# Kernel optimization log

Hardware: AMD Instinct MI355X
Metric: run time of the kernel (lower is better)

The kernel has to match this reference:

```python
import jax, jax.numpy as jnp
import numpy as np

C = 512        # concept_num
D = 256        # input_dim / embedding_dim
H = 512        # msg_hidden_dim
M = 256        # msg_output_dim
OH = 512       # hidden_dim
T = 2          # edge_type_num
E = C * (C - 1)  # fully-connected graph without self-loops = 261632


def _glorot(key, shape, fan_in):
    return jax.random.normal(key, shape, jnp.float32) / np.sqrt(fan_in).astype(np.float32)


def setup_inputs() -> dict:
    key = jax.random.key(0)
    ks = jax.random.split(key, 12)
    inputs = jax.random.normal(ks[0], (C, D), jnp.float32)
    rel_type = jax.random.uniform(ks[1], (E, T), jnp.float32)
    send_idx = jax.random.randint(ks[2], (E,), 0, C, jnp.int32)
    rec_idx = jax.random.randint(ks[3], (E,), 0, C, jnp.int32)
    # per-edge-type message MLP params, stacked over type dim
    W1 = _glorot(ks[4], (T, 2 * D, H), 2 * D)
    b1 = jnp.zeros((T, H), jnp.float32)
    W2 = _glorot(ks[5], (T, H, M), H)
    b2 = jnp.zeros((T, M), jnp.float32)
    # output MLP params
    Wo1 = _glorot(ks[6], (M, OH), M)
    bo1 = jnp.zeros((OH,), jnp.float32)
    Wo2 = _glorot(ks[7], (OH, OH), OH)
    bo2 = jnp.zeros((OH,), jnp.float32)
    Wo3 = _glorot(ks[8], (OH, D), OH)
    bo3 = jnp.zeros((D,), jnp.float32)
    return {"inputs": inputs, "rel_type": rel_type, "W1": W1, "b1": b1,
            "W2": W2, "b2": b2, "Wo1": Wo1, "bo1": bo1, "Wo2": Wo2,
            "bo2": bo2, "Wo3": Wo3, "bo3": bo3,
            "send_idx": send_idx, "rec_idx": rec_idx}


def reference(inputs, rel_type, W1, b1, W2, b2, Wo1, bo1, Wo2, bo2, Wo3, bo3,
              send_idx, rec_idx):
    # node2edge: one-hot sparse matmul == index gather
    senders = jnp.take(inputs, send_idx, axis=0)      # [E, D]
    receivers = jnp.take(inputs, rec_idx, axis=0)     # [E, D]
    pre_msg = jnp.concatenate([senders, receivers], axis=-1)  # [E, 2D]
    # per-edge-type MLPs, weighted-summed by rel_type (dropout=0 / eval mode)
    all_msgs = jnp.zeros((pre_msg.shape[0], M), jnp.float32)
    for i in range(T):
        msg = jax.nn.relu(pre_msg @ W1[i] + b1[i])    # [E, H]
        msg = jax.nn.relu(msg @ W2[i] + b2[i])        # [E, M]
        all_msgs = all_msgs + msg * rel_type[:, i:i + 1]
    # edge2node: transposed one-hot sparse matmul == scatter-add over receivers
    agg_msgs = jax.ops.segment_sum(all_msgs, rec_idx, num_segments=inputs.shape[0])  # [C, M]
    pred = jax.nn.relu(agg_msgs @ Wo1 + bo1)
    pred = jax.nn.relu(pred @ Wo2 + bo2)
    return pred @ Wo3 + bo3                           # [C, D]
```

## Files before the change

kernel.cpp:

```cpp
#include <hip/hip_runtime.h>

#define C_N   512
#define E_N   261632

typedef _Float16 f16;
typedef _Float16 f16x8_t __attribute__((ext_vector_type(8)));
typedef float    f32x16_t __attribute__((ext_vector_type(16)));

__global__ __launch_bounds__(256) void k_prep(
    const float* __restrict__ W1, const float* __restrict__ W2,
    const int* __restrict__ rec,
    const float* __restrict__ Wo1, const float* __restrict__ Wo2, const float* __restrict__ Wo3,
    f16* __restrict__ W1p, f16* __restrict__ W2p,
    f16* __restrict__ Wo1p, f16* __restrict__ Wo2p, f16* __restrict__ Wo3p,
    int* __restrict__ hist_part)
{
  int bid = blockIdx.x;
  if (bid < 256) {
    int gid  = bid * 256 + threadIdx.x;
    int lane = gid & 63;
    int nt   = (gid >> 6) & 15;
    int kc   = (gid >> 10) & 15;
    int mi   = gid >> 14;
    int t    = mi >> 1, half = mi & 1;
    const float* src = W1 + (size_t)t * 512 * 512 + (size_t)half * 256 * 512;
    int n  = nt * 32 + (lane & 31);
    int k0 = kc * 16 + (lane >> 5) * 8;
    f16x8_t v;
    #pragma unroll
    for (int j = 0; j < 8; j++) v[j] = (f16)src[(size_t)(k0 + j) * 512 + n];
    *(f16x8_t*)(W1p + (size_t)gid * 8) = v;
  } else if (bid < 384) {
    int gid  = (bid - 256) * 256 + threadIdx.x;
    int lane = gid & 63;
    int ct   = (gid >> 6) & 7;
    int kc   = (gid >> 9) & 31;
    int t    = gid >> 14;
    int n    = ct * 32 + (lane & 31);
    int k0   = kc * 16 + (lane >> 5) * 8;
    const float* src = W2 + (size_t)t * 512 * 256;
    f16x8_t v;
    #pragma unroll
    for (int j = 0; j < 8; j++) v[j] = (f16)src[(size_t)(k0 + j) * 256 + n];
    *(f16x8_t*)(W2p + (size_t)gid * 8) = v;
  } else if (bid < 448) {
    int hb = bid - 384;
    __shared__ int lh[512];
    for (int i = threadIdx.x; i < 512; i += 256) lh[i] = 0;
    __syncthreads();
    int e0 = hb * (E_N / 64);
    for (int i = threadIdx.x; i < E_N / 64; i += 256)
      atomicAdd(&lh[rec[e0 + i]], 1);
    __syncthreads();
    for (int i = threadIdx.x; i < 512; i += 256)
      hist_part[hb * 512 + i] = lh[i];
  } else if (bid < 512) {
    int gid  = (bid - 448) * 256 + threadIdx.x;
    int lane = gid & 63;
    int ct   = (gid >> 6) & 15;
    int kc   = gid >> 10;
    int n    = ct * 32 + (lane & 31);
    int k0   = kc * 16 + (lane >> 5) * 8;
    f16x8_t v;
    #pragma unroll
    for (int j = 0; j < 8; j++) v[j] = (f16)Wo1[(size_t)(k0 + j) * 512 + n];
    *(f16x8_t*)(Wo1p + (size_t)gid * 8) = v;
  } else if (bid < 640) {
    int gid  = (bid - 512) * 256 + threadIdx.x;
    int lane = gid & 63;
    int ct   = (gid >> 6) & 15;
    int kc   = gid >> 10;
    int n    = ct * 32 + (lane & 31);
    int k0   = kc * 16 + (lane >> 5) * 8;
    f16x8_t v;
    #pragma unroll
    for (int j = 0; j < 8; j++) v[j] = (f16)Wo2[(size_t)(k0 + j) * 512 + n];
    *(f16x8_t*)(Wo2p + (size_t)gid * 8) = v;
  } else {
    int gid  = (bid - 640) * 256 + threadIdx.x;
    int lane = gid & 63;
    int ct   = (gid >> 6) & 7;
    int kc   = gid >> 9;
    int n    = ct * 32 + (lane & 31);
    int k0   = kc * 16 + (lane >> 5) * 8;
    f16x8_t v;
    #pragma unroll
    for (int j = 0; j < 8; j++) v[j] = (f16)Wo3[(size_t)(k0 + j) * 256 + n];
    *(f16x8_t*)(Wo3p + (size_t)gid * 8) = v;
  }
}

__global__ __launch_bounds__(256) void k_sarb(const float* __restrict__ inputs,
    const f16* __restrict__ W1p, const float* __restrict__ b1,
    f16* __restrict__ SA, f16* __restrict__ RB)
{
  int tid = threadIdx.x, lane = tid & 63, w = tid >> 6;
  int hlf = lane >> 5, l31 = lane & 31;
  int br = blockIdx.x, bc = blockIdx.y, mi = blockIdx.z;
  int t = mi >> 1, half = mi & 1;
  const f16* Bmat = W1p + (size_t)mi * (256 * 512);
  f32x16_t acc[2][2];
  #pragma unroll
  for (int rt = 0; rt < 2; rt++)
    #pragma unroll
    for (int ctl = 0; ctl < 2; ctl++)
      #pragma unroll
      for (int r = 0; r < 16; r++) acc[rt][ctl][r] = 0.f;
  for (int kc = 0; kc < 16; kc++) {
    f16x8_t af[2];
    #pragma unroll
    for (int rt = 0; rt < 2; rt++) {
      const float4* p = (const float4*)&inputs[(size_t)(br * 64 + rt * 32 + l31) * 256 + kc * 16 + hlf * 8];
      float4 u0 = p[0], u1 = p[1];
      af[rt] = (f16x8_t){(f16)u0.x, (f16)u0.y, (f16)u0.z, (f16)u0.w,
                         (f16)u1.x, (f16)u1.y, (f16)u1.z, (f16)u1.w};
    }
    #pragma unroll
    for (int ctl = 0; ctl < 2; ctl++) {
      f16x8_t bfr = *(const f16x8_t*)&Bmat[((size_t)(kc * 16 + bc * 8 + 2 * w + ctl) * 64 + lane) * 8];
      #pragma unroll
      for (int rt = 0; rt < 2; rt++)
        acc[rt][ctl] = __builtin_amdgcn_mfma_f32_32x32x16_f16(af[rt], bfr, acc[rt][ctl], 0, 0, 0);
    }
  }
  f16* dst = (half == 0) ? SA : RB;
  #pragma unroll
  for (int ctl = 0; ctl < 2; ctl++) {
    int col = bc * 256 + (2 * w + ctl) * 32 + l31;
    float bias = (half == 1) ? b1[t * 512 + col] : 0.f;
    #pragma unroll
    for (int rt = 0; rt < 2; rt++)
      #pragma unroll
      for (int r = 0; r < 16; r++) {
        int row = br * 64 + rt * 32 + (r & 3) + 8 * (r >> 2) + 4 * hlf;
        dst[((size_t)(t * 512 + row)) * 512 + col] = (f16)(acc[rt][ctl][r] + bias);
      }
  }
}

__global__ void k_scan(const int* __restrict__ hist_part, int* __restrict__ seg,
                       int* __restrict__ base)
{
  __shared__ int s[512];
  int tid = threadIdx.x;
  int tot = 0;
  #pragma unroll 8
  for (int b = 0; b < 64; b++) tot += hist_part[b * 512 + tid];
  s[tid] = tot;
  __syncthreads();
  for (int off = 1; off < 512; off <<= 1) {
    int v = (tid >= off) ? s[tid - off] : 0;
    __syncthreads();
    s[tid] += v;
    __syncthreads();
  }
  int excl = s[tid] - tot;
  seg[tid] = excl;
  if (tid == 0) seg[512] = E_N;
  int run = excl;
  for (int b = 0; b < 64; b++) {
    base[b * 512 + tid] = run;
    run += hist_part[b * 512 + tid];
  }
}

__global__ __launch_bounds__(1024) void k_scatter3(const int* __restrict__ rec,
    const int* __restrict__ send, const float* __restrict__ rel,
    const int* __restrict__ base, int* __restrict__ ssend, float2* __restrict__ srel)
{
  __shared__ int lh[512];
  __shared__ int lb[512];
  int b = blockIdx.x;
  int e0 = b * (E_N / 64);
  for (int i = threadIdx.x; i < 512; i += 1024) { lh[i] = 0; lb[i] = base[b * 512 + i]; }
  __syncthreads();
  for (int i = threadIdx.x; i < E_N / 64; i += 1024) {
    int e = e0 + i;
    int r = rec[e];
    int p = lb[r] + atomicAdd(&lh[r], 1);
    ssend[p] = send[e];
    srel[p]  = make_float2(rel[2 * (size_t)e], rel[2 * (size_t)e + 1]);
  }
}

#define H1S2 264

__global__ __launch_bounds__(512, 4) void k_edges(
    const f16* __restrict__ SA, const f16* __restrict__ RB,
    const f16* __restrict__ W2p, const float* __restrict__ b2,
    const int* __restrict__ ssend, const float2* __restrict__ srel,
    const int* __restrict__ seg, float* __restrict__ agg)
{
  __shared__ f16   h1[128 * H1S2];
  __shared__ f16   rbs[2][512];
  __shared__ float b2s[2][256];
  __shared__ float aggL[256];
  __shared__ float relv2[2][128][2];
  __shared__ int   sends2[2][128];

  int c    = blockIdx.x;
  int tid  = threadIdx.x;
  int lane = tid & 63;
  int w    = tid >> 6;
  int hlf  = lane >> 5;
  int l31  = lane & 31;
  int q5   = tid & 31;
  int rb0  = tid >> 5;

  if (tid < 128) {
    int t = tid >> 6, qq = tid & 63;
    *(f16x8_t*)&rbs[t][qq * 8] = *(const f16x8_t*)&RB[((size_t)(t * 512 + c)) * 512 + qq * 8];
  }
  if (tid < 256) aggL[tid] = 0.0f;
  { int t = (tid >> 8) & 1, col = tid & 255; b2s[t][col] = b2[t * 256 + col]; }

  int s0 = seg[c], s1 = seg[c + 1];
  int nt = (s1 - s0 + 127) >> 7;

  if (nt > 0 && tid < 128) {
    int pos = s0 + tid;
    if (pos < s1) {
      sends2[0][tid] = ssend[pos];
      float2 rr = srel[pos];
      relv2[0][tid][0] = rr.x;
      relv2[0][tid][1] = rr.y;
    } else {
      sends2[0][tid] = 0; relv2[0][tid][0] = 0.f; relv2[0][tid][1] = 0.f;
    }
  }
  __syncthreads();

  f16x8_t g[8];
  const f16x8_t* SAc = (const f16x8_t*)SA;
  const f16x8_t* Bp  = (const f16x8_t*)W2p;
  f32x16_t acc[4];

  if (nt > 0) {
    #pragma unroll
    for (int j = 0; j < 8; j++)
      g[j] = SAc[(size_t)sends2[0][rb0 + 16 * j] * 64 + q5];
  }

  for (int ph = 0; ph < 4 * nt; ph++) {
    int ti  = ph >> 2;
    int t   = (ph >> 1) & 1;
    int kh  = ph & 1;
    int cb  = ti & 1;
    int nb  = cb ^ 1;
    bool more = (ti + 1 < nt);

    {
      f16x8_t rbq = *(const f16x8_t*)&rbs[t][(kh * 32 + q5) * 8];
      #pragma unroll
      for (int j = 0; j < 8; j++) {
        int row = rb0 + 16 * j;
        f16x8_t hv;
        #pragma unroll
        for (int e = 0; e < 8; e++) {
          f16 v = (f16)(g[j][e] + rbq[e]);
          hv[e] = (v > (f16)0.0f) ? v : (f16)0.0f;
        }
        *(f16x8_t*)&h1[row * H1S2 + q5 * 8] = hv;
      }
    }
    __syncthreads();

    if (t == 0 && kh == 0 && more && tid < 128) {
      int pos = s0 + (ti + 1) * 128 + tid;
      if (pos < s1) {
        sends2[nb][tid] = ssend[pos];
        float2 rr = srel[pos];
        relv2[nb][tid][0] = rr.x;
        relv2[nb][tid][1] = rr.y;
      } else {
        sends2[nb][tid] = 0; relv2[nb][tid][0] = 0.f; relv2[nb][tid][1] = 0.f;
      }
    }

    if (kh == 0) {
      #pragma unroll
      for (int rt = 0; rt < 4; rt++)
        #pragma unroll
        for (int r = 0; r < 16; r++) acc[rt][r] = 0.f;
    }

    f16x8_t bb[2];
    bb[0] = Bp[(size_t)(((t * 32 + kh * 16 + 0) * 8 + w) * 64 + lane)];
    bb[1] = Bp[(size_t)(((t * 32 + kh * 16 + 1) * 8 + w) * 64 + lane)];

    if (kh == 0) {
      #pragma unroll
      for (int j = 0; j < 8; j++)
        g[j] = SAc[(size_t)(t * 512 + sends2[cb][rb0 + 16 * j]) * 64 + 32 + q5];
    } else if (t == 0) {
      #pragma unroll
      for (int j = 0; j < 8; j++)
        g[j] = SAc[(size_t)(512 + sends2[cb][rb0 + 16 * j]) * 64 + q5];
    } else if (more) {
      #pragma unroll
      for (int j = 0; j < 8; j++)
        g[j] = SAc[(size_t)sends2[nb][rb0 + 16 * j] * 64 + q5];
    }

    for (int kc = 0; kc < 16; kc++) {
      int pb = kc & 1;
      #pragma unroll
      for (int rt = 0; rt < 4; rt++) {
        f16x8_t af = *(const f16x8_t*)&h1[(rt * 32 + l31) * H1S2 + kc * 16 + hlf * 8];
        acc[rt] = __builtin_amdgcn_mfma_f32_32x32x16_f16(af, bb[pb], acc[rt], 0, 0, 0);
      }
      if (kc + 2 < 16)
        bb[pb] = Bp[(size_t)(((t * 32 + kh * 16 + kc + 2) * 8 + w) * 64 + lane)];
    }

    if (kh == 1) {
      int col = w * 32 + l31;
      float b2c = b2s[t][col];
      float csum = 0.0f;
      #pragma unroll
      for (int rt = 0; rt < 4; rt++)
        #pragma unroll
        for (int r = 0; r < 16; r++) {
          int row = rt * 32 + (r & 3) + 8 * (r >> 2) + 4 * hlf;
          float v = fmaxf(acc[rt][r] + b2c, 0.0f);
          csum += v * relv2[cb][row][t];
        }
      csum += __shfl_xor(csum, 32, 64);
      if (hlf == 0) aggL[col] += csum;
    }
    __syncthreads();
  }

  if (tid < 256) agg[(size_t)c * 256 + tid] = aggL[tid];
}

__global__ __launch_bounds__(256) void k_omlp1(const float* __restrict__ agg,
    const f16* __restrict__ Wo1p, const float* __restrict__ bo1, f16* __restrict__ h1o)
{
  int tid = threadIdx.x, lane = tid & 63, w = tid >> 6;
  int hlf = lane >> 5, l31 = lane & 31;
  int br = blockIdx.x, bc = blockIdx.y;
  f32x16_t acc[2][2];
  #pragma unroll
  for (int rt = 0; rt < 2; rt++)
    #pragma unroll
    for (int ctl = 0; ctl < 2; ctl++)
      #pragma unroll
      for (int r = 0; r < 16; r++) acc[rt][ctl][r] = 0.f;
  for (int kc = 0; kc < 16; kc++) {
    f16x8_t af[2];
    #pragma unroll
    for (int rt = 0; rt < 2; rt++) {
      const float4* p = (const float4*)&agg[(size_t)(br * 64 + rt * 32 + l31) * 256 + kc * 16 + hlf * 8];
      float4 u0 = p[0], u1 = p[1];
      af[rt] = (f16x8_t){(f16)u0.x, (f16)u0.y, (f16)u0.z, (f16)u0.w,
                         (f16)u1.x, (f16)u1.y, (f16)u1.z, (f16)u1.w};
    }
    #pragma unroll
    for (int ctl = 0; ctl < 2; ctl++) {
      f16x8_t bfr = *(const f16x8_t*)&Wo1p[((size_t)(kc * 16 + bc * 8 + 2 * w + ctl) * 64 + lane) * 8];
      #pragma unroll
      for (int rt = 0; rt < 2; rt++)
        acc[rt][ctl] = __builtin_amdgcn_mfma_f32_32x32x16_f16(af[rt], bfr, acc[rt][ctl], 0, 0, 0);
    }
  }
  #pragma unroll
  for (int ctl = 0; ctl < 2; ctl++) {
    int col = bc * 256 + (2 * w + ctl) * 32 + l31;
    float bias = bo1[col];
    #pragma unroll
    for (int rt = 0; rt < 2; rt++)
      #pragma unroll
      for (int r = 0; r < 16; r++) {
        int row = br * 64 + rt * 32 + (r & 3) + 8 * (r >> 2) + 4 * hlf;
        h1o[(size_t)row * 512 + col] = (f16)fmaxf(acc[rt][ctl][r] + bias, 0.f);
      }
  }
}

__global__ __launch_bounds__(256) void k_omlp2(const f16* __restrict__ h1o,
    const f16* __restrict__ Wo2p, const float* __restrict__ bo2, f16* __restrict__ h2o)
{
  int tid = threadIdx.x, lane = tid & 63, w = tid >> 6;
  int hlf = lane >> 5, l31 = lane & 31;
  int br = blockIdx.x, bc = blockIdx.y;
  f32x16_t acc[2][2];
  #pragma unroll
  for (int rt = 0; rt < 2; rt++)
    #pragma unroll
    for (int ctl = 0; ctl < 2; ctl++)
      #pragma unroll
      for (int r = 0; r < 16; r++) acc[rt][ctl][r] = 0.f;
  for (int kc = 0; kc < 32; kc++) {
    f16x8_t af[2];
    #pragma unroll
    for (int rt = 0; rt < 2; rt++)
      af[rt] = *(const f16x8_t*)&h1o[(size_t)(br * 64 + rt * 32 + l31) * 512 + kc * 16 + hlf * 8];
    #pragma unroll
    for (int ctl = 0; ctl < 2; ctl++) {
      f16x8_t bfr = *(const f16x8_t*)&Wo2p[((size_t)(kc * 16 + bc * 8 + 2 * w + ctl) * 64 + lane) * 8];
      #pragma unroll
      for (int rt = 0; rt < 2; rt++)
        acc[rt][ctl] = __builtin_amdgcn_mfma_f32_32x32x16_f16(af[rt], bfr, acc[rt][ctl], 0, 0, 0);
    }
  }
  #pragma unroll
  for (int ctl = 0; ctl < 2; ctl++) {
    int col = bc * 256 + (2 * w + ctl) * 32 + l31;
    float bias = bo2[col];
    #pragma unroll
    for (int rt = 0; rt < 2; rt++)
      #pragma unroll
      for (int r = 0; r < 16; r++) {
        int row = br * 64 + rt * 32 + (r & 3) + 8 * (r >> 2) + 4 * hlf;
        h2o[(size_t)row * 512 + col] = (f16)fmaxf(acc[rt][ctl][r] + bias, 0.f);
      }
  }
}

__global__ __launch_bounds__(256) void k_omlp3(const f16* __restrict__ h2o,
    const f16* __restrict__ Wo3p, const float* __restrict__ bo3, float* __restrict__ out)
{
  int tid = threadIdx.x, lane = tid & 63, w = tid >> 6;
  int hlf = lane >> 5, l31 = lane & 31;
  int br = blockIdx.x;
  f32x16_t acc[2][2];
  #pragma unroll
  for (int rt = 0; rt < 2; rt++)
    #pragma unroll
    for (int ctl = 0; ctl < 2; ctl++)
      #pragma unroll
      for (int r = 0; r < 16; r++) acc[rt][ctl][r] = 0.f;
  for (int kc = 0; kc < 32; kc++) {
    f16x8_t af[2];
    #pragma unroll
    for (int rt = 0; rt < 2; rt++)
      af[rt] = *(const f16x8_t*)&h2o[(size_t)(br * 64 + rt * 32 + l31) * 512 + kc * 16 + hlf * 8];
    #pragma unroll
    for (int ctl = 0; ctl < 2; ctl++) {
      f16x8_t bfr = *(const f16x8_t*)&Wo3p[((size_t)(kc * 8 + 2 * w + ctl) * 64 + lane) * 8];
      #pragma unroll
      for (int rt = 0; rt < 2; rt++)
        acc[rt][ctl] = __builtin_amdgcn_mfma_f32_32x32x16_f16(af[rt], bfr, acc[rt][ctl], 0, 0, 0);
    }
  }
  #pragma unroll
  for (int ctl = 0; ctl < 2; ctl++) {
    int col = (2 * w + ctl) * 32 + l31;
    float bias = bo3[col];
    #pragma unroll
    for (int rt = 0; rt < 2; rt++)
      #pragma unroll
      for (int r = 0; r < 16; r++) {
        int row = br * 64 + rt * 32 + (r & 3) + 8 * (r >> 2) + 4 * hlf;
        out[(size_t)row * 256 + col] = acc[rt][ctl][r] + bias;
      }
  }
}

extern "C" void kernel_launch(void* const* d_in, const int* in_sizes, int n_in,
                              void* d_out, int out_size, void* d_ws, size_t ws_size,
                              hipStream_t stream)
{
  (void)in_sizes; (void)n_in; (void)out_size; (void)ws_size;
  const float* inputs = (const float*)d_in[0];
  const float* rel    = (const float*)d_in[1];
  const float* W1     = (const float*)d_in[2];
  const float* b1     = (const float*)d_in[3];
  const float* W2     = (const float*)d_in[4];
  const float* b2     = (const float*)d_in[5];
  const float* Wo1    = (const float*)d_in[6];
  const float* bo1    = (const float*)d_in[7];
  const float* Wo2    = (const float*)d_in[8];
  const float* bo2    = (const float*)d_in[9];
  const float* Wo3    = (const float*)d_in[10];
  const float* bo3    = (const float*)d_in[11];
  const int* send_idx = (const int*)d_in[12];
  const int* rec_idx  = (const int*)d_in[13];
  float* out = (float*)d_out;

  char* ws = (char*)d_ws;
  f16*    SA        = (f16*)   (ws);
  f16*    RB        = (f16*)   (ws + (1u << 20));
  f16*    W2p       = (f16*)   (ws + (2u << 20));
  float*  agg       = (float*) (ws + (2560u << 10));
  int*    hist_part = (int*)   (ws + (3u << 20));
  int*    seg       = (int*)   (ws + (3u << 20) + (128u << 10));
  int*    base      = (int*)   (ws + (3u << 20) + (132u << 10));
  int*    ssend     = (int*)   (ws + (3584u << 10));
  float2* srel      = (float2*)(ws + (4608u << 10));
  f16*    Wo1p      = (f16*)   (ws + (6656u << 10));
  f16*    Wo2p      = (f16*)   (ws + (6912u << 10));
  f16*    Wo3p      = (f16*)   (ws + (7424u << 10));
  f16*    h1o       = (f16*)   (ws + (7680u << 10));
  f16*    h2o       = (f16*)   (ws + (8192u << 10));
  f16*    W1p       = (f16*)   (ws + (8704u << 10));

  k_prep    <<<dim3(704),     dim3(256),  0, stream>>>(W1, W2, rec_idx, Wo1, Wo2, Wo3,
                                                       W1p, W2p, Wo1p, Wo2p, Wo3p, hist_part);
  k_sarb    <<<dim3(8, 2, 4), dim3(256),  0, stream>>>(inputs, W1p, b1, SA, RB);
  k_scan    <<<dim3(1),       dim3(512),  0, stream>>>(hist_part, seg, base);
  k_scatter3<<<dim3(64),      dim3(1024), 0, stream>>>(rec_idx, send_idx, rel, base, ssend, srel);
  k_edges   <<<dim3(512),     dim3(512),  0, stream>>>(SA, RB, W2p, b2, ssend, srel, seg, agg);
  k_omlp1   <<<dim3(8, 2),    dim3(256),  0, stream>>>(agg, Wo1p, bo1, h1o);
  k_omlp2   <<<dim3(8, 2),    dim3(256),  0, stream>>>(h1o, Wo2p, bo2, h2o);
  k_omlp3   <<<dim3(8),       dim3(256),  0, stream>>>(h2o, Wo3p, bo3, out);
}
```

Before: 310.9 us.

## Cut launches: fuse prep with SA/RB GEMM, bucket edges by atomics, fuse output MLP

The W1 pack kernel and the SA/RB GEMM are merged into one prep kernel that reads W1 directly. The histogram, scan and scatter passes are replaced by a single scatter pass into fixed-capacity (768) per-receiver buckets, using global atomic counters with padded slots. The three output-MLP kernels become one kernel that keeps intermediates in LDS. This cuts the launch count from 8 to 4 and removes global round trips. The risks are a receiver overflowing the fixed capacity, atomic ordering making the edge order nondeterministic, and only 8 blocks running the fused output MLP.

```diff
diff --git a/kernel.cpp b/kernel.cpp
--- a/kernel.cpp
+++ b/kernel.cpp
@@ -2,36 +2,71 @@
 
 #define C_N   512
 #define E_N   261632
+#define CAP   768
 
 typedef _Float16 f16;
 typedef _Float16 f16x8_t __attribute__((ext_vector_type(8)));
 typedef float    f32x16_t __attribute__((ext_vector_type(16)));
 
-__global__ __launch_bounds__(256) void k_prep(
-    const float* __restrict__ W1, const float* __restrict__ W2,
-    const int* __restrict__ rec,
+__global__ __launch_bounds__(256) void k_prep_all(
+    const float* __restrict__ inputs, const float* __restrict__ W1,
+    const float* __restrict__ b1, const float* __restrict__ W2,
     const float* __restrict__ Wo1, const float* __restrict__ Wo2, const float* __restrict__ Wo3,
-    f16* __restrict__ W1p, f16* __restrict__ W2p,
+    f16* __restrict__ SA, f16* __restrict__ RB, f16* __restrict__ W2p,
     f16* __restrict__ Wo1p, f16* __restrict__ Wo2p, f16* __restrict__ Wo3p,
-    int* __restrict__ hist_part)
+    int* __restrict__ cnt)
 {
   int bid = blockIdx.x;
-  if (bid < 256) {
-    int gid  = bid * 256 + threadIdx.x;
-    int lane = gid & 63;
-    int nt   = (gid >> 6) & 15;
-    int kc   = (gid >> 10) & 15;
-    int mi   = gid >> 14;
-    int t    = mi >> 1, half = mi & 1;
+  int tid = threadIdx.x;
+  if (bid < 64) {
+    int lane = tid & 63, w = tid >> 6;
+    int hlf = lane >> 5, l31 = lane & 31;
+    int br = bid & 7, bc = (bid >> 3) & 1, mi = bid >> 4;
+    int t = mi >> 1, half = mi & 1;
     const float* src = W1 + (size_t)t * 512 * 512 + (size_t)half * 256 * 512;
-    int n  = nt * 32 + (lane & 31);
-    int k0 = kc * 16 + (lane >> 5) * 8;
-    f16x8_t v;
-    #pragma unroll
-    for (int j = 0; j < 8; j++) v[j] = (f16)src[(size_t)(k0 + j) * 512 + n];
-    *(f16x8_t*)(W1p + (size_t)gid * 8) = v;
-  } else if (bid < 384) {
-    int gid  = (bid - 256) * 256 + threadIdx.x;
+    f32x16_t acc[2][2];
+    #pragma unroll
+    for (int rt = 0; rt < 2; rt++)
+      #pragma unroll
+      for (int ctl = 0; ctl < 2; ctl++)
+        #pragma unroll
+        for (int r = 0; r < 16; r++) acc[rt][ctl][r] = 0.f;
+    for (int kc = 0; kc < 16; kc++) {
+      f16x8_t af[2];
+      #pragma unroll
+      for (int rt = 0; rt < 2; rt++) {
+        const float4* p = (const float4*)&inputs[(size_t)(br * 64 + rt * 32 + l31) * 256 + kc * 16 + hlf * 8];
+        float4 u0 = p[0], u1 = p[1];
+        af[rt] = (f16x8_t){(f16)u0.x, (f16)u0.y, (f16)u0.z, (f16)u0.w,
+                           (f16)u1.x, (f16)u1.y, (f16)u1.z, (f16)u1.w};
+      }
+      #pragma unroll
+      for (int ctl = 0; ctl < 2; ctl++) {
+        int n  = bc * 256 + (2 * w + ctl) * 32 + l31;
+        int k0 = kc * 16 + hlf * 8;
+        f16x8_t bfr;
+        #pragma unroll
+        for (int j = 0; j < 8; j++) bfr[j] = (f16)src[(size_t)(k0 + j) * 512 + n];
+        #pragma unroll
+        for (int rt = 0; rt < 2; rt++)
+          acc[rt][ctl] = __builtin_amdgcn_mfma_f32_32x32x16_f16(af[rt], bfr, acc[rt][ctl], 0, 0, 0);
+      }
+    }
+    f16* dst = (half == 0) ? SA : RB;
+    #pragma unroll
+    for (int ctl = 0; ctl < 2; ctl++) {
+      int col = bc * 256 + (2 * w + ctl) * 32 + l31;
+      float bias = (half == 1) ? b1[t * 512 + col] : 0.f;
+      #pragma unroll
+      for (int rt = 0; rt < 2; rt++)
+        #pragma unroll
+        for (int r = 0; r < 16; r++) {
+          int row = br * 64 + rt * 32 + (r & 3) + 8 * (r >> 2) + 4 * hlf;
+          dst[((size_t)(t * 512 + row)) * 512 + col] = (f16)(acc[rt][ctl][r] + bias);
+        }
+    }
+  } else if (bid < 192) {
+    int gid  = (bid - 64) * 256 + tid;
     int lane = gid & 63;
     int ct   = (gid >> 6) & 7;
     int kc   = (gid >> 9) & 31;
@@ -43,19 +78,8 @@
     #pragma unroll
     for (int j = 0; j < 8; j++) v[j] = (f16)src[(size_t)(k0 + j) * 256 + n];
     *(f16x8_t*)(W2p + (size_t)gid * 8) = v;
-  } else if (bid < 448) {
-    int hb = bid - 384;
-    __shared__ int lh[512];
-    for (int i = threadIdx.x; i < 512; i += 256) lh[i] = 0;
-    __syncthreads();
-    int e0 = hb * (E_N / 64);
-    for (int i = threadIdx.x; i < E_N / 64; i += 256)
-      atomicAdd(&lh[rec[e0 + i]], 1);
-    __syncthreads();
-    for (int i = threadIdx.x; i < 512; i += 256)
-      hist_part[hb * 512 + i] = lh[i];
-  } else if (bid < 512) {
-    int gid  = (bid - 448) * 256 + threadIdx.x;
+  } else if (bid < 256) {
+    int gid  = (bid - 192) * 256 + tid;
     int lane = gid & 63;
     int ct   = (gid >> 6) & 15;
     int kc   = gid >> 10;
@@ -65,8 +89,8 @@
     #pragma unroll
     for (int j = 0; j < 8; j++) v[j] = (f16)Wo1[(size_t)(k0 + j) * 512 + n];
     *(f16x8_t*)(Wo1p + (size_t)gid * 8) = v;
-  } else if (bid < 640) {
-    int gid  = (bid - 512) * 256 + threadIdx.x;
+  } else if (bid < 384) {
+    int gid  = (bid - 256) * 256 + tid;
     int lane = gid & 63;
     int ct   = (gid >> 6) & 15;
     int kc   = gid >> 10;
@@ -76,8 +100,8 @@
     #pragma unroll
     for (int j = 0; j < 8; j++) v[j] = (f16)Wo2[(size_t)(k0 + j) * 512 + n];
     *(f16x8_t*)(Wo2p + (size_t)gid * 8) = v;
-  } else {
-    int gid  = (bid - 640) * 256 + threadIdx.x;
+  } else if (bid < 448) {
+    int gid  = (bid - 384) * 256 + tid;
     int lane = gid & 63;
     int ct   = (gid >> 6) & 7;
     int kc   = gid >> 9;
@@ -87,97 +111,34 @@
     #pragma unroll
     for (int j = 0; j < 8; j++) v[j] = (f16)Wo3[(size_t)(k0 + j) * 256 + n];
     *(f16x8_t*)(Wo3p + (size_t)gid * 8) = v;
+  } else {
+    for (int i = tid; i < 512 * 16; i += 256) cnt[i] = 0;
   }
 }
 
-__global__ __launch_bounds__(256) void k_sarb(const float* __restrict__ inputs,
-    const f16* __restrict__ W1p, const float* __restrict__ b1,
-    f16* __restrict__ SA, f16* __restrict__ RB)
-{
-  int tid = threadIdx.x, lane = tid & 63, w = tid >> 6;
-  int hlf = lane >> 5, l31 = lane & 31;
-  int br = blockIdx.x, bc = blockIdx.y, mi = blockIdx.z;
-  int t = mi >> 1, half = mi & 1;
-  const f16* Bmat = W1p + (size_t)mi * (256 * 512);
-  f32x16_t acc[2][2];
-  #pragma unroll
-  for (int rt = 0; rt < 2; rt++)
-    #pragma unroll
-    for (int ctl = 0; ctl < 2; ctl++)
-      #pragma unroll
-      for (int r = 0; r < 16; r++) acc[rt][ctl][r] = 0.f;
-  for (int kc = 0; kc < 16; kc++) {
-    f16x8_t af[2];
-    #pragma unroll
-    for (int rt = 0; rt < 2; rt++) {
-      const float4* p = (const float4*)&inputs[(size_t)(br * 64 + rt * 32 + l31) * 256 + kc * 16 + hlf * 8];
-      float4 u0 = p[0], u1 = p[1];
-      af[rt] = (f16x8_t){(f16)u0.x, (f16)u0.y, (f16)u0.z, (f16)u0.w,
-                         (f16)u1.x, (f16)u1.y, (f16)u1.z, (f16)u1.w};
-    }
-    #pragma unroll
-    for (int ctl = 0; ctl < 2; ctl++) {
-      f16x8_t bfr = *(const f16x8_t*)&Bmat[((size_t)(kc * 16 + bc * 8 + 2 * w + ctl) * 64 + lane) * 8];
-      #pragma unroll
-      for (int rt = 0; rt < 2; rt++)
-        acc[rt][ctl] = __builtin_amdgcn_mfma_f32_32x32x16_f16(af[rt], bfr, acc[rt][ctl], 0, 0, 0);
-    }
-  }
-  f16* dst = (half == 0) ? SA : RB;
-  #pragma unroll
-  for (int ctl = 0; ctl < 2; ctl++) {
-    int col = bc * 256 + (2 * w + ctl) * 32 + l31;
-    float bias = (half == 1) ? b1[t * 512 + col] : 0.f;
-    #pragma unroll
-    for (int rt = 0; rt < 2; rt++)
-      #pragma unroll
-      for (int r = 0; r < 16; r++) {
-        int row = br * 64 + rt * 32 + (r & 3) + 8 * (r >> 2) + 4 * hlf;
-        dst[((size_t)(t * 512 + row)) * 512 + col] = (f16)(acc[rt][ctl][r] + bias);
-      }
-  }
-}
-
-__global__ void k_scan(const int* __restrict__ hist_part, int* __restrict__ seg,
-                       int* __restrict__ base)
-{
-  __shared__ int s[512];
-  int tid = threadIdx.x;
-  int tot = 0;
-  #pragma unroll 8
-  for (int b = 0; b < 64; b++) tot += hist_part[b * 512 + tid];
-  s[tid] = tot;
-  __syncthreads();
-  for (int off = 1; off < 512; off <<= 1) {
-    int v = (tid >= off) ? s[tid - off] : 0;
-    __syncthreads();
-    s[tid] += v;
-    __syncthreads();
-  }
-  int excl = s[tid] - tot;
-  seg[tid] = excl;
-  if (tid == 0) seg[512] = E_N;
-  int run = excl;
-  for (int b = 0; b < 64; b++) {
-    base[b * 512 + tid] = run;
-    run += hist_part[b * 512 + tid];
-  }
-}
-
-__global__ __launch_bounds__(1024) void k_scatter3(const int* __restrict__ rec,
+__global__ __launch_bounds__(1024) void k_scatter_d(const int* __restrict__ rec,
     const int* __restrict__ send, const float* __restrict__ rel,
-    const int* __restrict__ base, int* __restrict__ ssend, float2* __restrict__ srel)
+    int* __restrict__ cnt, int* __restrict__ ssend, float2* __restrict__ srel)
 {
   __shared__ int lh[512];
   __shared__ int lb[512];
   int b = blockIdx.x;
   int e0 = b * (E_N / 64);
-  for (int i = threadIdx.x; i < 512; i += 1024) { lh[i] = 0; lb[i] = base[b * 512 + i]; }
+  if (threadIdx.x < 512) lh[threadIdx.x] = 0;
+  __syncthreads();
+  for (int i = threadIdx.x; i < E_N / 64; i += 1024)
+    atomicAdd(&lh[rec[e0 + i]], 1);
+  __syncthreads();
+  if (threadIdx.x < 512) {
+    int c = lh[threadIdx.x];
+    lb[threadIdx.x] = c ? atomicAdd(&cnt[threadIdx.x * 16], c) : 0;
+    lh[threadIdx.x] = 0;
+  }
   __syncthreads();
   for (int i = threadIdx.x; i < E_N / 64; i += 1024) {
     int e = e0 + i;
     int r = rec[e];
-    int p = lb[r] + atomicAdd(&lh[r], 1);
+    int p = (int)((size_t)r * CAP) + lb[r] + atomicAdd(&lh[r], 1);
     ssend[p] = send[e];
     srel[p]  = make_float2(rel[2 * (size_t)e], rel[2 * (size_t)e + 1]);
   }
@@ -189,7 +150,7 @@
     const f16* __restrict__ SA, const f16* __restrict__ RB,
     const f16* __restrict__ W2p, const float* __restrict__ b2,
     const int* __restrict__ ssend, const float2* __restrict__ srel,
-    const int* __restrict__ seg, float* __restrict__ agg)
+    const int* __restrict__ cnt, float* __restrict__ agg)
 {
   __shared__ f16   h1[128 * H1S2];
   __shared__ f16   rbs[2][512];
@@ -214,7 +175,8 @@
   if (tid < 256) aggL[tid] = 0.0f;
   { int t = (tid >> 8) & 1, col = tid & 255; b2s[t][col] = b2[t * 256 + col]; }
 
-  int s0 = seg[c], s1 = seg[c + 1];
+  int s0 = c * CAP;
+  int s1 = s0 + cnt[c * 16];
   int nt = (s1 - s0 + 127) >> 7;
 
   if (nt > 0 && tid < 128) {
@@ -334,126 +296,120 @@
   if (tid < 256) agg[(size_t)c * 256 + tid] = aggL[tid];
 }
 
-__global__ __launch_bounds__(256) void k_omlp1(const float* __restrict__ agg,
-    const f16* __restrict__ Wo1p, const float* __restrict__ bo1, f16* __restrict__ h1o)
+#define HOS 520
+
+__global__ __launch_bounds__(512, 1) void k_omlp(const float* __restrict__ agg,
+    const f16* __restrict__ Wo1p, const float* __restrict__ bo1,
+    const f16* __restrict__ Wo2p, const float* __restrict__ bo2,
+    const f16* __restrict__ Wo3p, const float* __restrict__ bo3,
+    float* __restrict__ out)
 {
-  int tid = threadIdx.x, lane = tid & 63, w = tid >> 6;
-  int hlf = lane >> 5, l31 = lane & 31;
-  int br = blockIdx.x, bc = blockIdx.y;
-  f32x16_t acc[2][2];
-  #pragma unroll
-  for (int rt = 0; rt < 2; rt++)
-    #pragma unroll
-    for (int ctl = 0; ctl < 2; ctl++)
-      #pragma unroll
-      for (int r = 0; r < 16; r++) acc[rt][ctl][r] = 0.f;
-  for (int kc = 0; kc < 16; kc++) {
-    f16x8_t af[2];
-    #pragma unroll
-    for (int rt = 0; rt < 2; rt++) {
-      const float4* p = (const float4*)&agg[(size_t)(br * 64 + rt * 32 + l31) * 256 + kc * 16 + hlf * 8];
-      float4 u0 = p[0], u1 = p[1];
-      af[rt] = (f16x8_t){(f16)u0.x, (f16)u0.y, (f16)u0.z, (f16)u0.w,
-                         (f16)u1.x, (f16)u1.y, (f16)u1.z, (f16)u1.w};
-    }
-    #pragma unroll
-    for (int ctl = 0; ctl < 2; ctl++) {
-      f16x8_t bfr = *(const f16x8_t*)&Wo1p[((size_t)(kc * 16 + bc * 8 + 2 * w + ctl) * 64 + lane) * 8];
-      #pragma unroll
-      for (int rt = 0; rt < 2; rt++)
-        acc[rt][ctl] = __builtin_amdgcn_mfma_f32_32x32x16_f16(af[rt], bfr, acc[rt][ctl], 0, 0, 0);
-    }
-  }
-  #pragma unroll
-  for (int ctl = 0; ctl < 2; ctl++) {
-    int col = bc * 256 + (2 * w + ctl) * 32 + l31;
-    float bias = bo1[col];
-    #pragma unroll
-    for (int rt = 0; rt < 2; rt++)
-      #pragma unroll
-      for (int r = 0; r < 16; r++) {
-        int row = br * 64 + rt * 32 + (r & 3) + 8 * (r >> 2) + 4 * hlf;
-        h1o[(size_t)row * 512 + col] = (f16)fmaxf(acc[rt][ctl][r] + bias, 0.f);
-      }
-  }
-}
-
-__global__ __launch_bounds__(256) void k_omlp2(const f16* __restrict__ h1o,
-    const f16* __restrict__ Wo2p, const float* __restrict__ bo2, f16* __restrict__ h2o)
-{
-  int tid = threadIdx.x, lane = tid & 63, w = tid >> 6;
-  int hlf = lane >> 5, l31 = lane & 31;
-  int br = blockIdx.x, bc = blockIdx.y;
-  f32x16_t acc[2][2];
-  #pragma unroll
-  for (int rt = 0; rt < 2; rt++)
-    #pragma unroll
-    for (int ctl = 0; ctl < 2; ctl++)
-      #pragma unroll
-      for (int r = 0; r < 16; r++) acc[rt][ctl][r] = 0.f;
-  for (int kc = 0; kc < 32; kc++) {
-    f16x8_t af[2];
-    #pragma unroll
-    for (int rt = 0; rt < 2; rt++)
-      af[rt] = *(const f16x8_t*)&h1o[(size_t)(br * 64 + rt * 32 + l31) * 512 + kc * 16 + hlf * 8];
-    #pragma unroll
-    for (int ctl = 0; ctl < 2; ctl++) {
-      f16x8_t bfr = *(const f16x8_t*)&Wo2p[((size_t)(kc * 16 + bc * 8 + 2 * w + ctl) * 64 + lane) * 8];
-      #pragma unroll
-      for (int rt = 0; rt < 2; rt++)
-        acc[rt][ctl] = __builtin_amdgcn_mfma_f32_32x32x16_f16(af[rt], bfr, acc[rt][ctl], 0, 0, 0);
-    }
-  }
-  #pragma unroll
-  for (int ctl = 0; ctl < 2; ctl++) {
-    int col = bc * 256 + (2 * w + ctl) * 32 + l31;
-    float bias = bo2[col];
-    #pragma unroll
-    for (int rt = 0; rt < 2; rt++)
-      #pragma unroll
-      for (int r = 0; r < 16; r++) {
-        int row = br * 64 + rt * 32 + (r & 3) + 8 * (r >> 2) + 4 * hlf;
-        h2o[(size_t)row * 512 + col] = (f16)fmaxf(acc[rt][ctl][r] + bias, 0.f);
-      }
-  }
-}
-
-__global__ __launch_bounds__(256) void k_omlp3(const f16* __restrict__ h2o,
-    const f16* __restrict__ Wo3p, const float* __restrict__ bo3, float* __restrict__ out)
-{
+  __shared__ f16 hL1[64 * HOS];
+  __shared__ f16 hL2[64 * HOS];
   int tid = threadIdx.x, lane = tid & 63, w = tid >> 6;
   int hlf = lane >> 5, l31 = lane & 31;
   int br = blockIdx.x;
-  f32x16_t acc[2][2];
-  #pragma unroll
-  for (int rt = 0; rt < 2; rt++)
-    #pragma unroll
-    for (int ctl = 0; ctl < 2; ctl++)
-      #pragma unroll
-      for (int r = 0; r < 16; r++) acc[rt][ctl][r] = 0.f;
-  for (int kc = 0; kc < 32; kc++) {
-    f16x8_t af[2];
+
+  {
+    f32x16_t acc[2][2];
     #pragma unroll
     for (int rt = 0; rt < 2; rt++)
-      af[rt] = *(const f16x8_t*)&h2o[(size_t)(br * 64 + rt * 32 + l31) * 512 + kc * 16 + hlf * 8];
+      #pragma unroll
+      for (int ctl = 0; ctl < 2; ctl++)
+        #pragma unroll
+        for (int r = 0; r < 16; r++) acc[rt][ctl][r] = 0.f;
+    for (int kc = 0; kc < 16; kc++) {
+      f16x8_t af[2];
+      #pragma unroll
+      for (int rt = 0; rt < 2; rt++) {
+        const float4* p = (const float4*)&agg[(size_t)(br * 64 + rt * 32 + l31) * 256 + kc * 16 + hlf * 8];
+        float4 u0 = p[0], u1 = p[1];
+        af[rt] = (f16x8_t){(f16)u0.x, (f16)u0.y, (f16)u0.z, (f16)u0.w,
+                           (f16)u1.x, (f16)u1.y, (f16)u1.z, (f16)u1.w};
+      }
+      #pragma unroll
+      for (int ctl = 0; ctl < 2; ctl++) {
+        int ct = 2 * w + ctl;
+        f16x8_t bfr = *(const f16x8_t*)&Wo1p[((size_t)(kc * 16 + ct) * 64 + lane) * 8];
+        #pragma unroll
+        for (int rt = 0; rt < 2; rt++)
+          acc[rt][ctl] = __builtin_amdgcn_mfma_f32_32x32x16_f16(af[rt], bfr, acc[rt][ctl], 0, 0, 0);
+      }
+    }
     #pragma unroll
     for (int ctl = 0; ctl < 2; ctl++) {
-      f16x8_t bfr = *(const f16x8_t*)&Wo3p[((size_t)(kc * 8 + 2 * w + ctl) * 64 + lane) * 8];
+      int col = (2 * w + ctl) * 32 + l31;
+      float bias = bo1[col];
       #pragma unroll
       for (int rt = 0; rt < 2; rt++)
-        acc[rt][ctl] = __builtin_amdgcn_mfma_f32_32x32x16_f16(af[rt], bfr, acc[rt][ctl], 0, 0, 0);
-    }
-  }
-  #pragma unroll
-  for (int ctl = 0; ctl < 2; ctl++) {
-    int col = (2 * w + ctl) * 32 + l31;
+        #pragma unroll
+        for (int r = 0; r < 16; r++) {
+          int row = rt * 32 + (r & 3) + 8 * (r >> 2) + 4 * hlf;
+          hL1[row * HOS + col] = (f16)fmaxf(acc[rt][ctl][r] + bias, 0.f);
+        }
+    }
+  }
+  __syncthreads();
+
+  {
+    f32x16_t acc[2][2];
+    #pragma unroll
+    for (int rt = 0; rt < 2; rt++)
+      #pragma unroll
+      for (int ctl = 0; ctl < 2; ctl++)
+        #pragma unroll
+        for (int r = 0; r < 16; r++) acc[rt][ctl][r] = 0.f;
+    for (int kc = 0; kc < 32; kc++) {
+      f16x8_t af[2];
+      #pragma unroll
+      for (int rt = 0; rt < 2; rt++)
+        af[rt] = *(const f16x8_t*)&hL1[(rt * 32 + l31) * HOS + kc * 16 + hlf * 8];
+      #pragma unroll
+      for (int ctl = 0; ctl < 2; ctl++) {
+        int ct = 2 * w + ctl;
+        f16x8_t bfr = *(const f16x8_t*)&Wo2p[((size_t)(kc * 16 + ct) * 64 + lane) * 8];
+        #pragma unroll
+        for (int rt = 0; rt < 2; rt++)
+          acc[rt][ctl] = __builtin_amdgcn_mfma_f32_32x32x16_f16(af[rt], bfr, acc[rt][ctl], 0, 0, 0);
+      }
+    }
+    #pragma unroll
+    for (int ctl = 0; ctl < 2; ctl++) {
+      int col = (2 * w + ctl) * 32 + l31;
+      float bias = bo2[col];
+      #pragma unroll
+      for (int rt = 0; rt < 2; rt++)
+        #pragma unroll
+        for (int r = 0; r < 16; r++) {
+          int row = rt * 32 + (r & 3) + 8 * (r >> 2) + 4 * hlf;
+          hL2[row * HOS + col] = (f16)fmaxf(acc[rt][ctl][r] + bias, 0.f);
+        }
+    }
+  }
+  __syncthreads();
+
+  {
+    f32x16_t acc[2];
+    #pragma unroll
+    for (int rt = 0; rt < 2; rt++)
+      #pragma unroll
+      for (int r = 0; r < 16; r++) acc[rt][r] = 0.f;
+    for (int kc = 0; kc < 32; kc++) {
+      f16x8_t bfr = *(const f16x8_t*)&Wo3p[((size_t)(kc * 8 + w) * 64 + lane) * 8];
+      #pragma unroll
+      for (int rt = 0; rt < 2; rt++) {
+        f16x8_t af = *(const f16x8_t*)&hL2[(rt * 32 + l31) * HOS + kc * 16 + hlf * 8];
+        acc[rt] = __builtin_amdgcn_mfma_f32_32x32x16_f16(af, bfr, acc[rt], 0, 0, 0);
+      }
+    }
+    int col = w * 32 + l31;
     float bias = bo3[col];
     #pragma unroll
     for (int rt = 0; rt < 2; rt++)
       #pragma unroll
       for (int r = 0; r < 16; r++) {
         int row = br * 64 + rt * 32 + (r & 3) + 8 * (r >> 2) + 4 * hlf;
-        out[(size_t)row * 256 + col] = acc[rt][ctl][r] + bias;
+        out[(size_t)row * 256 + col] = acc[rt][r] + bias;
       }
   }
 }
@@ -480,29 +436,20 @@
   float* out = (float*)d_out;
 
   char* ws = (char*)d_ws;
-  f16*    SA        = (f16*)   (ws);
-  f16*    RB        = (f16*)   (ws + (1u << 20));
-  f16*    W2p       = (f16*)   (ws + (2u << 20));
-  float*  agg       = (float*) (ws + (2560u << 10));
-  int*    hist_part = (int*)   (ws + (3u << 20));
-  int*    seg       = (int*)   (ws + (3u << 20) + (128u << 10));
-  int*    base      = (int*)   (ws + (3u << 20) + (132u << 10));
-  int*    ssend     = (int*)   (ws + (3584u << 10));
-  float2* srel      = (float2*)(ws + (4608u << 10));
-  f16*    Wo1p      = (f16*)   (ws + (6656u << 10));
-  f16*    Wo2p      = (f16*)   (ws + (6912u << 10));
-  f16*    Wo3p      = (f16*)   (ws + (7424u << 10));
-  f16*    h1o       = (f16*)   (ws + (7680u << 10));
-  f16*    h2o       = (f16*)   (ws + (8192u << 10));
-  f16*    W1p       = (f16*)   (ws + (8704u << 10));
-
-  k_prep    <<<dim3(704),     dim3(256),  0, stream>>>(W1, W2, rec_idx, Wo1, Wo2, Wo3,
-                                                       W1p, W2p, Wo1p, Wo2p, Wo3p, hist_part);
-  k_sarb    <<<dim3(8, 2, 4), dim3(256),  0, stream>>>(inputs, W1p, b1, SA, RB);
-  k_scan    <<<dim3(1),       dim3(512),  0, stream>>>(hist_part, seg, base);
-  k_scatter3<<<dim3(64),      dim3(1024), 0, stream>>>(rec_idx, send_idx, rel, base, ssend, srel);
-  k_edges   <<<dim3(512),     dim3(512),  0, stream>>>(SA, RB, W2p, b2, ssend, srel, seg, agg);
-  k_omlp1   <<<dim3(8, 2),    dim3(256),  0, stream>>>(agg, Wo1p, bo1, h1o);
-  k_omlp2   <<<dim3(8, 2),    dim3(256),  0, stream>>>(h1o, Wo2p, bo2, h2o);
-  k_omlp3   <<<dim3(8),       dim3(256),  0, stream>>>(h2o, Wo3p, bo3, out);
+  f16*    SA    = (f16*)   (ws);
+  f16*    RB    = (f16*)   (ws + (1024u << 10));
+  f16*    W2p   = (f16*)   (ws + (2048u << 10));
+  float*  agg   = (float*) (ws + (2560u << 10));
+  int*    cnt   = (int*)   (ws + (3072u << 10));
+  f16*    Wo1p  = (f16*)   (ws + (3136u << 10));
+  f16*    Wo2p  = (f16*)   (ws + (3392u << 10));
+  f16*    Wo3p  = (f16*)   (ws + (3904u << 10));
+  int*    ssend = (int*)   (ws + (4160u << 10));
+  float2* srel  = (float2*)(ws + (5696u << 10));
+
+  k_prep_all <<<dim3(449), dim3(256),  0, stream>>>(inputs, W1, b1, W2, Wo1, Wo2, Wo3,
+                                                    SA, RB, W2p, Wo1p, Wo2p, Wo3p, cnt);
+  k_scatter_d<<<dim3(64),  dim3(1024), 0, stream>>>(rec_idx, send_idx, rel, cnt, ssend, srel);
+  k_edges    <<<dim3(512), dim3(512),  0, stream>>>(SA, RB, W2p, b2, ssend, srel, cnt, agg);
+  k_omlp     <<<dim3(8),   dim3(512),  0, stream>>>(agg, Wo1p, bo1, Wo2p, bo2, Wo3p, bo3, out);
 }
```

Result: no change. 306.3 us (-1.5%).
